# Kernel tuning notes

Measured on AMD Instinct MI355X. Metric: run time of the kernel, lower is better.

Reference implementation:

```python
import jax, jax.numpy as jnp
import numpy as np

N_INST = 50000
D_IN, D_HID, D_ATT = 1024, 512, 256  # size_dict['small']
N_ENS = 4
N_CLS = 2
CB_SIZE = 256
BETA = 0.25
TOP_K = 1


def setup_inputs() -> dict:
    key = jax.random.key(0)
    ks = jax.random.split(key, 9)
    h = jax.random.normal(ks[0], (N_INST, D_IN), dtype=jnp.float32)
    fc_W = jax.random.normal(ks[1], (D_IN, D_HID), dtype=jnp.float32) * (1.0 / np.sqrt(D_IN))
    fc_b = jnp.zeros((D_HID,), dtype=jnp.float32)
    Ua = jax.random.normal(ks[2], (N_ENS, D_HID, D_ATT), dtype=jnp.float32) * (1.0 / np.sqrt(D_HID))
    Ub = jax.random.normal(ks[3], (N_ENS, D_HID, D_ATT), dtype=jnp.float32) * (1.0 / np.sqrt(D_HID))
    Uc = jax.random.normal(ks[4], (N_ENS, D_ATT, 1), dtype=jnp.float32) * (1.0 / np.sqrt(D_ATT))
    cls_W = jax.random.normal(ks[5], (D_HID, N_CLS), dtype=jnp.float32) * (1.0 / np.sqrt(D_HID))
    cls_b = jnp.zeros((N_CLS,), dtype=jnp.float32)
    codebook = jax.random.normal(ks[6], (CB_SIZE, D_HID), dtype=jnp.float32)
    return {"h": h, "fc_W": fc_W, "fc_b": fc_b, "Ua": Ua, "Ub": Ub,
            "Uc": Uc, "cls_W": cls_W, "cls_b": cls_b, "codebook": codebook}


def _vector_quantization(M, codebook):
    # NOTE: original code uses +2*matmul (sign bug in torch source); kept faithful.
    dist = (jnp.sum(M * M, axis=1, keepdims=True)
            + jnp.sum(codebook * codebook, axis=1)
            + 2.0 * (M @ codebook.T))                      # [1, CB]
    inds = jnp.argmin(dist, axis=1)                        # [1]
    one_hot = jax.nn.one_hot(inds, CB_SIZE, dtype=M.dtype)  # [1, CB]
    q = one_hot @ codebook                                  # [1, D_HID]
    commitment = jnp.mean((jax.lax.stop_gradient(q) - M) ** 2)
    embedding = jnp.mean((q - jax.lax.stop_gradient(M)) ** 2)
    vq_loss = commitment * BETA + embedding
    q_st = M + jax.lax.stop_gradient(q - M)  # straight-through (unused downstream)
    return vq_loss, q_st


def reference(h, fc_W, fc_b, Ua, Ub, Uc, cls_W, cls_b, codebook):
    # fc + ReLU: [n, D_HID]
    x = jax.nn.relu(h @ fc_W + fc_b)
    # gated batch-ensemble attention (ensemble dim n=4 broadcast)
    xe = jnp.broadcast_to(x[None], (N_ENS, x.shape[0], D_HID))
    a = jnp.tanh(jnp.einsum('ndk,nkl->ndl', xe, Ua))         # [4, n, D_ATT]
    b = jax.nn.sigmoid(jnp.einsum('ndk,nkl->ndl', xe, Ub))   # [4, n, D_ATT]
    A = jnp.einsum('ndk,nkl->ndl', a * b, Uc).sum(0)          # [n, 1]
    A = jax.nn.sigmoid(A.T)                                   # [1, n]
    M = (A @ x) / jnp.sum(A)                                  # [1, D_HID]
    vq_loss, _M_code = _vector_quantization(M, codebook)
    logits = M @ cls_W + cls_b                                # [1, N_CLS]
    y_probs = jax.nn.softmax(logits, axis=1)
    _, top_idx = jax.lax.top_k(y_probs[:, 1], TOP_K)          # [1]
    top_instance = logits[top_idx]                            # [1, N_CLS]
    Y_hat = jnp.argmax(top_instance, axis=1)[:, None]         # [1, 1] int
    Y_prob = jax.nn.softmax(top_instance, axis=1)
    return (top_instance, Y_prob, Y_hat, vq_loss, y_probs, A)
```

## Files before the change

kernel.cpp:

```cpp
#include <hip/hip_runtime.h>
#include <hip/hip_bf16.h>
#include <math.h>

typedef __bf16 bf16_t;
typedef __bf16 bf16x8 __attribute__((ext_vector_type(8)));
typedef float  f32x4  __attribute__((ext_vector_type(4)));

#define MINST 50000

typedef const __attribute__((address_space(1))) void* gas1_t;
typedef __attribute__((address_space(3))) void* las3_t;
__device__ __forceinline__ void gload16(const void* g, const void* l){
  __builtin_amdgcn_global_load_lds((gas1_t)g, (las3_t)l, 16, 0, 0);
}

__device__ __forceinline__ float fast_sigmoid(float x){
  return __fdividef(1.f, 1.f + __expf(-x));
}
__device__ __forceinline__ float fast_tanh(float x){
  float e = __expf(2.f*x);
  return 1.f - __fdividef(2.f, e + 1.f);
}

__global__ void prep_wt(const float* __restrict__ W, bf16_t* __restrict__ WT){
  int idx = blockIdx.x*256 + threadIdx.x;
  if (idx >= 512*1024) return;
  int n = idx >> 10, k = idx & 1023;
  WT[idx] = (bf16_t)W[k*512 + n];
}

__global__ void prep_uab(const float* __restrict__ Ua, const float* __restrict__ Ub,
                         bf16_t* __restrict__ UabT){
  int idx = blockIdx.x*256 + threadIdx.x;
  if (idx >= 2048*512) return;
  int c = idx >> 9, k = idx & 511;
  int s = c & 1, t = c >> 1;
  int n = t >> 8, l = t & 255;
  const float* src = s ? Ub : Ua;
  UabT[idx] = (bf16_t)src[(n*512 + k)*256 + l];
}

__global__ void zero_ws_k(float* __restrict__ Alogit, float* __restrict__ Mbuf){
  int i = blockIdx.x*256 + threadIdx.x;
  if (i < MINST) Alogit[i] = 0.f;
  if (i < 513)   Mbuf[i]  = 0.f;
}

template<int EPI, int K, int NBY>
__global__ __launch_bounds__(256, 2)
void gemm_k(const void* __restrict__ Ap, const bf16_t* __restrict__ Bp, int M,
            const float* __restrict__ bias, bf16_t* __restrict__ Xout,
            const float* __restrict__ Uc, float* __restrict__ Alogit)
{
  __shared__ bf16_t As[(EPI==0?1:2)][128*32] __attribute__((aligned(16)));
  __shared__ bf16_t Bs[2][128*32] __attribute__((aligned(16)));

  const int tid  = threadIdx.x;
  const int lane = tid & 63;
  const int w    = tid >> 6;
  const int wr   = w >> 1;
  const int wc   = w & 1;

  const int nwg = gridDim.x;
  const int q = nwg >> 3, r = nwg & 7;
  const int x = blockIdx.x & 7, pos = blockIdx.x >> 3;
  const int logical = (x < r ? x*(q+1) : r*(q+1) + (x-r)*q) + pos;
  const int m0 = (logical / NBY) * 128;
  const int n0 = (logical % NBY) * 128;

  const f32x4 fzero = {0.f, 0.f, 0.f, 0.f};
  f32x4 acc[4][4];
#pragma unroll
  for (int m = 0; m < 4; ++m)
#pragma unroll
    for (int n = 0; n < 4; ++n) acc[m][n] = fzero;

  const int srow = lane >> 2;
  const int schk = (lane & 3) * 8;
  const bf16_t* bsrc0 = Bp + (size_t)(n0 + w*32 + srow)*K + schk;
  const bf16_t* bsrc1 = bsrc0 + (size_t)16*K;

  auto stageB = [&](int buf, int k0){
    gload16(bsrc0 + k0, &Bs[buf][(w*32     )*32]);
    gload16(bsrc1 + k0, &Bs[buf][(w*32 + 16)*32]);
  };

  const bf16_t* asrc0 = (const bf16_t*)Ap + (size_t)(m0 + w*32 + srow)*K + schk;
  const bf16_t* asrc1 = asrc0 + (size_t)16*K;
  auto stageA1 = [&](int buf, int k0){
    gload16(asrc0 + k0, &As[buf][(w*32     )*32]);
    gload16(asrc1 + k0, &As[buf][(w*32 + 16)*32]);
  };

  const int a_row  = tid >> 1;
  const int a_half = tid & 1;
  f32x4 sAf[4];
  auto loadA0 = [&](int k0){
    const float* A = (const float*)Ap;
    int gr = m0 + a_row;
    if (gr < M) {
      const f32x4* p = (const f32x4*)(A + (size_t)gr*K + k0 + a_half*16);
      sAf[0]=p[0]; sAf[1]=p[1]; sAf[2]=p[2]; sAf[3]=p[3];
    } else {
      sAf[0]=fzero; sAf[1]=fzero; sAf[2]=fzero; sAf[3]=fzero;
    }
  };
  auto writeA0 = [&](){
    bf16x8 lo, hi;
#pragma unroll
    for (int j = 0; j < 4; ++j) {
      lo[j]   = (bf16_t)sAf[0][j];
      lo[4+j] = (bf16_t)sAf[1][j];
      hi[j]   = (bf16_t)sAf[2][j];
      hi[4+j] = (bf16_t)sAf[3][j];
    }
    *(bf16x8*)&As[0][a_row*32 + a_half*16    ] = lo;
    *(bf16x8*)&As[0][a_row*32 + a_half*16 + 8] = hi;
  };

  const int fr = lane & 15;
  const int kh = lane >> 4;
  constexpr int NT = K / 32;

  if constexpr (EPI == 0) {
    loadA0(0);
    stageB(0, 0);
#pragma unroll 4
    for (int kt = 0; kt < NT; ++kt) {
      const int cur = kt & 1;
      __syncthreads();
      writeA0();
      __syncthreads();
      if (kt + 1 < NT) { loadA0((kt+1)*32); stageB(cur^1, (kt+1)*32); }
      bf16x8 a[4], b[4];
#pragma unroll
      for (int m = 0; m < 4; ++m)
        a[m] = *(const bf16x8*)&As[0][(wr*64 + m*16 + fr)*32 + kh*8];
#pragma unroll
      for (int n = 0; n < 4; ++n)
        b[n] = *(const bf16x8*)&Bs[cur][(wc*64 + n*16 + fr)*32 + kh*8];
#pragma unroll
      for (int m = 0; m < 4; ++m)
#pragma unroll
        for (int n = 0; n < 4; ++n)
          acc[m][n] = __builtin_amdgcn_mfma_f32_16x16x32_bf16(a[m], b[n], acc[m][n], 0, 0, 0);
    }
  } else {
    stageA1(0, 0);
    stageB(0, 0);
#pragma unroll 4
    for (int kt = 0; kt < NT; ++kt) {
      const int cur = kt & 1;
      __syncthreads();
      if (kt + 1 < NT) { stageA1(cur^1, (kt+1)*32); stageB(cur^1, (kt+1)*32); }
      bf16x8 a[4], b[4];
#pragma unroll
      for (int m = 0; m < 4; ++m)
        a[m] = *(const bf16x8*)&As[cur][(wr*64 + m*16 + fr)*32 + kh*8];
#pragma unroll
      for (int n = 0; n < 4; ++n)
        b[n] = *(const bf16x8*)&Bs[cur][(wc*64 + n*16 + fr)*32 + kh*8];
#pragma unroll
      for (int m = 0; m < 4; ++m)
#pragma unroll
        for (int n = 0; n < 4; ++n)
          acc[m][n] = __builtin_amdgcn_mfma_f32_16x16x32_bf16(a[m], b[n], acc[m][n], 0, 0, 0);
    }
  }

  const int rg = lane >> 4;
  if constexpr (EPI == 0) {
#pragma unroll
    for (int n = 0; n < 4; ++n) {
      int col = n0 + wc*64 + n*16 + fr;
      float bv = bias[col];
#pragma unroll
      for (int m = 0; m < 4; ++m)
#pragma unroll
        for (int rr = 0; rr < 4; ++rr) {
          int row = m0 + wr*64 + m*16 + rg*4 + rr;
          if (row < M) {
            float v = acc[m][n][rr] + bv;
            Xout[(size_t)row*512 + col] = (bf16_t)(v > 0.f ? v : 0.f);
          }
        }
    }
  } else {
    float gacc[4][4];
#pragma unroll
    for (int m = 0; m < 4; ++m)
#pragma unroll
      for (int rr = 0; rr < 4; ++rr) gacc[m][rr] = 0.f;
    const bool even = (lane & 1) == 0;
#pragma unroll
    for (int n = 0; n < 4; ++n) {
      int col = n0 + wc*64 + n*16 + fr;
      float ucv = Uc[col >> 1];
#pragma unroll
      for (int m = 0; m < 4; ++m)
#pragma unroll
        for (int rr = 0; rr < 4; ++rr) {
          float v = acc[m][n][rr];
          float tv = even ? fast_tanh(v) : fast_sigmoid(v);
          float pv = __shfl_xor(tv, 1);
          gacc[m][rr] += tv * pv * ucv;
        }
    }
#pragma unroll
    for (int m = 0; m < 4; ++m)
#pragma unroll
      for (int rr = 0; rr < 4; ++rr) {
        float s = gacc[m][rr];
        s += __shfl_xor(s, 1);
        s += __shfl_xor(s, 2);
        s += __shfl_xor(s, 4);
        s += __shfl_xor(s, 8);
        if (fr == 0) {
          int row = m0 + wr*64 + m*16 + rg*4 + rr;
          if (row < M) atomicAdd(&Alogit[row], 0.5f * s);
        }
      }
  }
}

__global__ void a_final(const float* __restrict__ Alogit, float* __restrict__ outA,
                        float* __restrict__ sumA){
  int i = blockIdx.x*256 + threadIdx.x;
  float a = 0.f;
  if (i < MINST) { a = fast_sigmoid(Alogit[i]); outA[i] = a; }
  float s = a;
#pragma unroll
  for (int o = 1; o < 64; o <<= 1) s += __shfl_xor(s, o);
  __shared__ float wsum[4];
  int lane = threadIdx.x & 63, w = threadIdx.x >> 6;
  if (lane == 0) wsum[w] = s;
  __syncthreads();
  if (threadIdx.x == 0) atomicAdd(sumA, wsum[0]+wsum[1]+wsum[2]+wsum[3]);
}

__global__ void m_reduce(const bf16_t* __restrict__ Xb, const float* __restrict__ Aout,
                         float* __restrict__ Mbuf){
  int t = threadIdx.x;
  int c0 = (t & 63) * 8;
  float acc[8];
#pragma unroll
  for (int j = 0; j < 8; ++j) acc[j] = 0.f;
  for (int r = blockIdx.x*4 + (t>>6); r < MINST; r += gridDim.x*4) {
    float a = Aout[r];
    bf16x8 xv = *(const bf16x8*)(Xb + (size_t)r*512 + c0);
#pragma unroll
    for (int j = 0; j < 8; ++j) acc[j] += a * (float)xv[j];
  }
#pragma unroll
  for (int j = 0; j < 8; ++j) atomicAdd(&Mbuf[c0 + j], acc[j]);
}

__device__ __forceinline__ float block_sum256(float v, float* red){
  int t = threadIdx.x;
  red[t] = v; __syncthreads();
  for (int s = 128; s > 0; s >>= 1) {
    if (t < s) red[t] += red[t+s];
    __syncthreads();
  }
  float rr = red[0];
  __syncthreads();
  return rr;
}

__global__ __launch_bounds__(256)
void finalize_k(const float* __restrict__ Mbuf, const float* __restrict__ cb,
                const float* __restrict__ clsW, const float* __restrict__ clsb,
                float* __restrict__ dout)
{
  __shared__ float Mn[512];
  __shared__ float red[256];
  __shared__ float dist[256];
  __shared__ int   idxs[256];
  __shared__ int   indS;
  int t = threadIdx.x;
  float sA = Mbuf[512];
  Mn[t]     = Mbuf[t]     / sA;
  Mn[t+256] = Mbuf[t+256] / sA;
  __syncthreads();
  float msq_p = Mn[t]*Mn[t] + Mn[t+256]*Mn[t+256];
  float Msq = block_sum256(msq_p, red);

  const float* cbr = cb + t*512;
  float cs = 0.f, dt = 0.f;
  for (int k = 0; k < 512; k += 4) {
    f32x4 c = *(const f32x4*)(cbr + k);
    cs += c[0]*c[0] + c[1]*c[1] + c[2]*c[2] + c[3]*c[3];
    dt += Mn[k]*c[0] + Mn[k+1]*c[1] + Mn[k+2]*c[2] + Mn[k+3]*c[3];
  }
  dist[t] = Msq + cs + 2.f*dt;
  idxs[t] = t;
  __syncthreads();
  for (int s = 128; s > 0; s >>= 1) {
    if (t < s && dist[t+s] < dist[t]) { dist[t] = dist[t+s]; idxs[t] = idxs[t+s]; }
    __syncthreads();
  }
  if (t == 0) indS = idxs[0];
  __syncthreads();

  const float* qv = cb + (size_t)indS*512;
  float d0 = qv[t]     - Mn[t];
  float d1 = qv[t+256] - Mn[t+256];
  float vqs = block_sum256(d0*d0 + d1*d1, red);
  float vq_loss = 1.25f * (vqs / 512.f);

  float p0 = Mn[t]*clsW[t*2]   + Mn[t+256]*clsW[(t+256)*2];
  float p1 = Mn[t]*clsW[t*2+1] + Mn[t+256]*clsW[(t+256)*2+1];
  float l0 = block_sum256(p0, red);
  float l1 = block_sum256(p1, red);

  if (t == 0) {
    l0 += clsb[0]; l1 += clsb[1];
    float mx = fmaxf(l0, l1);
    float e0 = __expf(l0 - mx), e1 = __expf(l1 - mx);
    float si = e0 + e1;
    float y0 = e0 / si, y1 = e1 / si;
    int yhat = (l1 > l0) ? 1 : 0;
    dout[0] = l0; dout[1] = l1;
    dout[2] = y0; dout[3] = y1;
    dout[4] = (float)yhat;
    dout[5] = vq_loss;
    dout[6] = y0; dout[7] = y1;
  }
}

extern "C" void kernel_launch(void* const* d_in, const int* in_sizes, int n_in,
                              void* d_out, int out_size, void* d_ws, size_t ws_size,
                              hipStream_t stream) {
  const float* h    = (const float*)d_in[0];
  const float* fcW  = (const float*)d_in[1];
  const float* fcb  = (const float*)d_in[2];
  const float* Ua   = (const float*)d_in[3];
  const float* Ub   = (const float*)d_in[4];
  const float* Uc   = (const float*)d_in[5];
  const float* clsW = (const float*)d_in[6];
  const float* clsb = (const float*)d_in[7];
  const float* cbk  = (const float*)d_in[8];
  float* out = (float*)d_out;

  char* ws = (char*)d_ws;
  bf16_t* Xb     = (bf16_t*)ws;
  bf16_t* WT     = (bf16_t*)(ws + 51200000);
  bf16_t* UabT   = (bf16_t*)(ws + 52248576);
  float*  Alogit = (float*)(ws + 54345728);
  float*  Mbuf   = (float*)(ws + 54545728);

  const int M = MINST;

  prep_wt <<<2048, 256, 0, stream>>>(fcW, WT);
  prep_uab<<<4096, 256, 0, stream>>>(Ua, Ub, UabT);
  zero_ws_k<<<196, 256, 0, stream>>>(Alogit, Mbuf);

  gemm_k<0,1024,4><<<1564, 256, 0, stream>>>(h, WT, M, fcb, Xb, nullptr, nullptr);
  gemm_k<1, 512,16><<<6256, 256, 0, stream>>>(Xb, UabT, M, nullptr, nullptr, Uc, Alogit);

  a_final <<<196, 256, 0, stream>>>(Alogit, out + 8, Mbuf + 512);
  m_reduce<<<128, 256, 0, stream>>>(Xb, out + 8, Mbuf);
  finalize_k<<<1, 256, 0, stream>>>(Mbuf, cbk, clsW, clsb, out);
}
```

Measured before the change: 507.1 us.

## Use 64-wide K tiles with XOR-swizzled LDS layout in GEMM kernels

Doubles the K-step of each shared-memory tile from 32 to 64, halving the number of loop iterations and barriers, and applies an XOR swizzle on 16-byte chunks to avoid LDS bank conflicts when reading fragments. For the attention GEMM (EPI!=0) it replaces double buffering with a single buffer that is read into registers and then refilled, and it drops the unroll pragmas. The risk is more registers for doubled fragments and less load/compute overlap in the single-buffered path.

```diff
diff --git a/kernel.cpp b/kernel.cpp
--- a/kernel.cpp
+++ b/kernel.cpp
@@ -52,8 +52,9 @@
             const float* __restrict__ bias, bf16_t* __restrict__ Xout,
             const float* __restrict__ Uc, float* __restrict__ Alogit)
 {
-  __shared__ bf16_t As[(EPI==0?1:2)][128*32] __attribute__((aligned(16)));
-  __shared__ bf16_t Bs[2][128*32] __attribute__((aligned(16)));
+  constexpr int NBUFB = (EPI==0 ? 2 : 1);
+  __shared__ bf16_t As[128*64] __attribute__((aligned(16)));
+  __shared__ bf16_t Bs[NBUFB][128*64] __attribute__((aligned(16)));
 
   const int tid  = threadIdx.x;
   const int lane = tid & 63;
@@ -75,96 +76,109 @@
 #pragma unroll
     for (int n = 0; n < 4; ++n) acc[m][n] = fzero;
 
-  const int srow = lane >> 2;
-  const int schk = (lane & 3) * 8;
-  const bf16_t* bsrc0 = Bp + (size_t)(n0 + w*32 + srow)*K + schk;
-  const bf16_t* bsrc1 = bsrc0 + (size_t)16*K;
-
-  auto stageB = [&](int buf, int k0){
-    gload16(bsrc0 + k0, &Bs[buf][(w*32     )*32]);
-    gload16(bsrc1 + k0, &Bs[buf][(w*32 + 16)*32]);
-  };
-
-  const bf16_t* asrc0 = (const bf16_t*)Ap + (size_t)(m0 + w*32 + srow)*K + schk;
-  const bf16_t* asrc1 = asrc0 + (size_t)16*K;
-  auto stageA1 = [&](int buf, int k0){
-    gload16(asrc0 + k0, &As[buf][(w*32     )*32]);
-    gload16(asrc1 + k0, &As[buf][(w*32 + 16)*32]);
+  const int sR = lane >> 3;
+  const int sC = (lane & 7) ^ sR;
+
+  auto stageB = [&](int kt, int buf){
+#pragma unroll
+    for (int j = 0; j < 4; ++j) {
+      int rL = w*32 + j*8;
+      gload16(Bp + (size_t)(n0 + rL + sR)*K + kt*64 + sC*8, &Bs[buf][rL*64]);
+    }
+  };
+  auto stageA1 = [&](int kt){
+    const bf16_t* Ab = (const bf16_t*)Ap;
+#pragma unroll
+    for (int j = 0; j < 4; ++j) {
+      int rL = w*32 + j*8;
+      gload16(Ab + (size_t)(m0 + rL + sR)*K + kt*64 + sC*8, &As[rL*64]);
+    }
   };
 
   const int a_row  = tid >> 1;
   const int a_half = tid & 1;
-  f32x4 sAf[4];
-  auto loadA0 = [&](int k0){
+  f32x4 sAf[8];
+  auto loadA0 = [&](int kt){
     const float* A = (const float*)Ap;
     int gr = m0 + a_row;
     if (gr < M) {
-      const f32x4* p = (const f32x4*)(A + (size_t)gr*K + k0 + a_half*16);
-      sAf[0]=p[0]; sAf[1]=p[1]; sAf[2]=p[2]; sAf[3]=p[3];
+      const f32x4* p = (const f32x4*)(A + (size_t)gr*K + kt*64 + a_half*32);
+#pragma unroll
+      for (int j = 0; j < 8; ++j) sAf[j] = p[j];
     } else {
-      sAf[0]=fzero; sAf[1]=fzero; sAf[2]=fzero; sAf[3]=fzero;
+#pragma unroll
+      for (int j = 0; j < 8; ++j) sAf[j] = fzero;
     }
   };
   auto writeA0 = [&](){
-    bf16x8 lo, hi;
 #pragma unroll
     for (int j = 0; j < 4; ++j) {
-      lo[j]   = (bf16_t)sAf[0][j];
-      lo[4+j] = (bf16_t)sAf[1][j];
-      hi[j]   = (bf16_t)sAf[2][j];
-      hi[4+j] = (bf16_t)sAf[3][j];
-    }
-    *(bf16x8*)&As[0][a_row*32 + a_half*16    ] = lo;
-    *(bf16x8*)&As[0][a_row*32 + a_half*16 + 8] = hi;
+      bf16x8 v;
+#pragma unroll
+      for (int e = 0; e < 4; ++e) { v[e] = (bf16_t)sAf[2*j][e]; v[4+e] = (bf16_t)sAf[2*j+1][e]; }
+      int c = (a_half*4 + j) ^ (a_row & 7);
+      *(bf16x8*)&As[a_row*64 + c*8] = v;
+    }
   };
 
   const int fr = lane & 15;
   const int kh = lane >> 4;
-  constexpr int NT = K / 32;
+  auto readFrags = [&](int buf, bf16x8 (&a)[4][2], bf16x8 (&b)[4][2]){
+#pragma unroll
+    for (int m = 0; m < 4; ++m){
+      int R = wr*64 + m*16 + fr;
+#pragma unroll
+      for (int ks = 0; ks < 2; ++ks){
+        int c = ((ks<<2)|kh) ^ (R & 7);
+        a[m][ks] = *(const bf16x8*)&As[R*64 + c*8];
+      }
+    }
+#pragma unroll
+    for (int n = 0; n < 4; ++n){
+      int R = wc*64 + n*16 + fr;
+#pragma unroll
+      for (int ks = 0; ks < 2; ++ks){
+        int c = ((ks<<2)|kh) ^ (R & 7);
+        b[n][ks] = *(const bf16x8*)&Bs[buf][R*64 + c*8];
+      }
+    }
+  };
+
+  constexpr int NT = K / 64;
 
   if constexpr (EPI == 0) {
-    loadA0(0);
-    stageB(0, 0);
-#pragma unroll 4
+    loadA0(0); stageB(0, 0);
     for (int kt = 0; kt < NT; ++kt) {
       const int cur = kt & 1;
       __syncthreads();
       writeA0();
       __syncthreads();
-      if (kt + 1 < NT) { loadA0((kt+1)*32); stageB(cur^1, (kt+1)*32); }
-      bf16x8 a[4], b[4];
-#pragma unroll
-      for (int m = 0; m < 4; ++m)
-        a[m] = *(const bf16x8*)&As[0][(wr*64 + m*16 + fr)*32 + kh*8];
-#pragma unroll
-      for (int n = 0; n < 4; ++n)
-        b[n] = *(const bf16x8*)&Bs[cur][(wc*64 + n*16 + fr)*32 + kh*8];
-#pragma unroll
-      for (int m = 0; m < 4; ++m)
-#pragma unroll
-        for (int n = 0; n < 4; ++n)
-          acc[m][n] = __builtin_amdgcn_mfma_f32_16x16x32_bf16(a[m], b[n], acc[m][n], 0, 0, 0);
+      if (kt + 1 < NT) { loadA0(kt+1); stageB(kt+1, cur^1); }
+      bf16x8 a[4][2], b[4][2];
+      readFrags(cur, a, b);
+#pragma unroll
+      for (int ks = 0; ks < 2; ++ks)
+#pragma unroll
+        for (int m = 0; m < 4; ++m)
+#pragma unroll
+          for (int n = 0; n < 4; ++n)
+            acc[m][n] = __builtin_amdgcn_mfma_f32_16x16x32_bf16(a[m][ks], b[n][ks], acc[m][n], 0, 0, 0);
     }
   } else {
-    stageA1(0, 0);
-    stageB(0, 0);
-#pragma unroll 4
+    stageA1(0); stageB(0, 0);
     for (int kt = 0; kt < NT; ++kt) {
-      const int cur = kt & 1;
       __syncthreads();
-      if (kt + 1 < NT) { stageA1(cur^1, (kt+1)*32); stageB(cur^1, (kt+1)*32); }
-      bf16x8 a[4], b[4];
-#pragma unroll
-      for (int m = 0; m < 4; ++m)
-        a[m] = *(const bf16x8*)&As[cur][(wr*64 + m*16 + fr)*32 + kh*8];
-#pragma unroll
-      for (int n = 0; n < 4; ++n)
-        b[n] = *(const bf16x8*)&Bs[cur][(wc*64 + n*16 + fr)*32 + kh*8];
-#pragma unroll
-      for (int m = 0; m < 4; ++m)
-#pragma unroll
-        for (int n = 0; n < 4; ++n)
-          acc[m][n] = __builtin_amdgcn_mfma_f32_16x16x32_bf16(a[m], b[n], acc[m][n], 0, 0, 0);
+      bf16x8 a[4][2], b[4][2];
+      readFrags(0, a, b);
+      __syncthreads();
+      if (kt + 1 < NT) { stageA1(kt+1); stageB(kt+1, 0); }
+#pragma unroll
+      for (int ks = 0; ks < 2; ++ks)
+#pragma unroll
+        for (int m = 0; m < 4; ++m)
+#pragma unroll
+          for (int n = 0; n < 4; ++n)
+            acc[m][n] = __builtin_amdgcn_mfma_f32_16x16x32_bf16(a[m][ks], b[n][ks], acc[m][n], 0, 0, 0);
     }
   }
 
```

After: 505.9 us. Within noise of the previous version (-0.3%).

## Split GEMM into specialized kernels with async fp32 A staging and swizzled LDS

Applied to the files above, without the earlier changes.

The templated GEMM is split into two kernels. The fc GEMM now streams fp32 activations straight into double-buffered LDS with global_load_lds and converts them to bf16 at fragment-read time, replacing the register load, convert and store path that needed two barriers per k-step. Both kernels get XOR-swizzled LDS layouts to cut bank conflicts, a single barrier per iteration, and higher occupancy hints (3 and 5 blocks per CU). The fp32 A tile doubles LDS use in the fc kernel and adds per-fragment conversion work, and the higher occupancy targets may raise register pressure.

```diff
diff --git a/kernel.cpp b/kernel.cpp
--- a/kernel.cpp
+++ b/kernel.cpp
@@ -46,14 +46,13 @@
   if (i < 513)   Mbuf[i]  = 0.f;
 }
 
-template<int EPI, int K, int NBY>
-__global__ __launch_bounds__(256, 2)
-void gemm_k(const void* __restrict__ Ap, const bf16_t* __restrict__ Bp, int M,
-            const float* __restrict__ bias, bf16_t* __restrict__ Xout,
-            const float* __restrict__ Uc, float* __restrict__ Alogit)
+__global__ __launch_bounds__(256, 3)
+void gemm_fc(const float* __restrict__ Ap, const bf16_t* __restrict__ Bp, int M,
+             const float* __restrict__ bias, bf16_t* __restrict__ Xout)
 {
-  __shared__ bf16_t As[(EPI==0?1:2)][128*32] __attribute__((aligned(16)));
-  __shared__ bf16_t Bs[2][128*32] __attribute__((aligned(16)));
+  constexpr int K = 1024, NBY = 4, NT = K/32;
+  __shared__ float  Asf[2][128*32] __attribute__((aligned(16)));
+  __shared__ bf16_t Bs [2][128*32] __attribute__((aligned(16)));
 
   const int tid  = threadIdx.x;
   const int lane = tid & 63;
@@ -75,152 +74,184 @@
 #pragma unroll
     for (int n = 0; n < 4; ++n) acc[m][n] = fzero;
 
-  const int srow = lane >> 2;
-  const int schk = (lane & 3) * 8;
-  const bf16_t* bsrc0 = Bp + (size_t)(n0 + w*32 + srow)*K + schk;
-  const bf16_t* bsrc1 = bsrc0 + (size_t)16*K;
-
-  auto stageB = [&](int buf, int k0){
-    gload16(bsrc0 + k0, &Bs[buf][(w*32     )*32]);
-    gload16(bsrc1 + k0, &Bs[buf][(w*32 + 16)*32]);
+  const int sq8 = lane >> 3;
+  const int sc8 = (lane & 7) ^ sq8;
+  const float* aSrc[4];
+#pragma unroll
+  for (int j = 0; j < 4; ++j){
+    int srow = m0 + w*32 + j*8 + sq8;
+    if (srow > M-1) srow = M-1;
+    aSrc[j] = Ap + (size_t)srow*K + sc8*4;
+  }
+  const int sq4 = lane >> 2;
+  const int sc4 = (lane & 3) ^ ((sq4 + (sq4 >> 2)) & 3);
+  const bf16_t* bSrc[2];
+#pragma unroll
+  for (int j = 0; j < 2; ++j)
+    bSrc[j] = Bp + (size_t)(n0 + w*32 + j*16 + sq4)*K + sc4*8;
+
+  auto stage = [&](int kt, int buf){
+#pragma unroll
+    for (int j = 0; j < 4; ++j)
+      gload16(aSrc[j] + kt*32, &Asf[buf][(w*32 + j*8)*32]);
+#pragma unroll
+    for (int j = 0; j < 2; ++j)
+      gload16(bSrc[j] + kt*32, &Bs[buf][(w*32 + j*16)*32]);
   };
 
-  const bf16_t* asrc0 = (const bf16_t*)Ap + (size_t)(m0 + w*32 + srow)*K + schk;
-  const bf16_t* asrc1 = asrc0 + (size_t)16*K;
-  auto stageA1 = [&](int buf, int k0){
-    gload16(asrc0 + k0, &As[buf][(w*32     )*32]);
-    gload16(asrc1 + k0, &As[buf][(w*32 + 16)*32]);
-  };
-
-  const int a_row  = tid >> 1;
-  const int a_half = tid & 1;
-  f32x4 sAf[4];
-  auto loadA0 = [&](int k0){
-    const float* A = (const float*)Ap;
-    int gr = m0 + a_row;
-    if (gr < M) {
-      const f32x4* p = (const f32x4*)(A + (size_t)gr*K + k0 + a_half*16);
-      sAf[0]=p[0]; sAf[1]=p[1]; sAf[2]=p[2]; sAf[3]=p[3];
-    } else {
-      sAf[0]=fzero; sAf[1]=fzero; sAf[2]=fzero; sAf[3]=fzero;
+  const int fr = lane & 15;
+  const int kh = lane >> 4;
+  const int cb = (kh ^ ((fr + (fr >> 2)) & 3)) * 8;
+  const int ca0 = ((2*kh    ) ^ (fr & 7)) * 4;
+  const int ca1 = ((2*kh + 1) ^ (fr & 7)) * 4;
+
+  stage(0, 0);
+  __syncthreads();
+  for (int kt = 0; kt < NT; ++kt){
+    const int cur = kt & 1;
+    if (kt + 1 < NT) stage(kt+1, cur^1);
+    bf16x8 a[4], b[4];
+#pragma unroll
+    for (int m = 0; m < 4; ++m){
+      int R = wr*64 + m*16 + fr;
+      f32x4 lo = *(const f32x4*)&Asf[cur][R*32 + ca0];
+      f32x4 hi = *(const f32x4*)&Asf[cur][R*32 + ca1];
+#pragma unroll
+      for (int e = 0; e < 4; ++e){ a[m][e] = (bf16_t)lo[e]; a[m][4+e] = (bf16_t)hi[e]; }
+    }
+#pragma unroll
+    for (int n = 0; n < 4; ++n)
+      b[n] = *(const bf16x8*)&Bs[cur][(wc*64 + n*16 + fr)*32 + cb];
+#pragma unroll
+    for (int m = 0; m < 4; ++m)
+#pragma unroll
+      for (int n = 0; n < 4; ++n)
+        acc[m][n] = __builtin_amdgcn_mfma_f32_16x16x32_bf16(a[m], b[n], acc[m][n], 0, 0, 0);
+    __syncthreads();
+  }
+
+  const int rg = lane >> 4;
+#pragma unroll
+  for (int n = 0; n < 4; ++n) {
+    int col = n0 + wc*64 + n*16 + fr;
+    float bv = bias[col];
+#pragma unroll
+    for (int m = 0; m < 4; ++m)
+#pragma unroll
+      for (int rr = 0; rr < 4; ++rr) {
+        int row = m0 + wr*64 + m*16 + rg*4 + rr;
+        if (row < M) {
+          float v = acc[m][n][rr] + bv;
+          Xout[(size_t)row*512 + col] = (bf16_t)(v > 0.f ? v : 0.f);
+        }
+      }
+  }
+}
+
+__global__ __launch_bounds__(256, 5)
+void gemm_att(const bf16_t* __restrict__ Xb, const bf16_t* __restrict__ Bp, int M,
+              const float* __restrict__ Uc, float* __restrict__ Alogit)
+{
+  constexpr int K = 512, NBY = 16, NT = K/32;
+  __shared__ bf16_t As[2][128*32] __attribute__((aligned(16)));
+  __shared__ bf16_t Bs[2][128*32] __attribute__((aligned(16)));
+
+  const int tid  = threadIdx.x;
+  const int lane = tid & 63;
+  const int w    = tid >> 6;
+  const int wr   = w >> 1;
+  const int wc   = w & 1;
+
+  const int nwg = gridDim.x;
+  const int q = nwg >> 3, r = nwg & 7;
+  const int x = blockIdx.x & 7, pos = blockIdx.x >> 3;
+  const int logical = (x < r ? x*(q+1) : r*(q+1) + (x-r)*q) + pos;
+  const int m0 = (logical / NBY) * 128;
+  const int n0 = (logical % NBY) * 128;
+
+  const f32x4 fzero = {0.f, 0.f, 0.f, 0.f};
+  f32x4 acc[4][4];
+#pragma unroll
+  for (int m = 0; m < 4; ++m)
+#pragma unroll
+    for (int n = 0; n < 4; ++n) acc[m][n] = fzero;
+
+  const int sq = lane >> 2;
+  const int sc = (lane & 3) ^ ((sq + (sq >> 2)) & 3);
+  const bf16_t* aSrc[2]; const bf16_t* bSrc[2];
+#pragma unroll
+  for (int j = 0; j < 2; ++j){
+    int rL = w*32 + j*16;
+    aSrc[j] = Xb + (size_t)(m0 + rL + sq)*K + sc*8;
+    bSrc[j] = Bp + (size_t)(n0 + rL + sq)*K + sc*8;
+  }
+  auto stage = [&](int kt, int buf){
+#pragma unroll
+    for (int j = 0; j < 2; ++j){
+      gload16(aSrc[j] + kt*32, &As[buf][(w*32 + j*16)*32]);
+      gload16(bSrc[j] + kt*32, &Bs[buf][(w*32 + j*16)*32]);
     }
   };
-  auto writeA0 = [&](){
-    bf16x8 lo, hi;
-#pragma unroll
-    for (int j = 0; j < 4; ++j) {
-      lo[j]   = (bf16_t)sAf[0][j];
-      lo[4+j] = (bf16_t)sAf[1][j];
-      hi[j]   = (bf16_t)sAf[2][j];
-      hi[4+j] = (bf16_t)sAf[3][j];
-    }
-    *(bf16x8*)&As[0][a_row*32 + a_half*16    ] = lo;
-    *(bf16x8*)&As[0][a_row*32 + a_half*16 + 8] = hi;
-  };
 
   const int fr = lane & 15;
   const int kh = lane >> 4;
-  constexpr int NT = K / 32;
-
-  if constexpr (EPI == 0) {
-    loadA0(0);
-    stageB(0, 0);
-#pragma unroll 4
-    for (int kt = 0; kt < NT; ++kt) {
-      const int cur = kt & 1;
-      __syncthreads();
-      writeA0();
-      __syncthreads();
-      if (kt + 1 < NT) { loadA0((kt+1)*32); stageB(cur^1, (kt+1)*32); }
-      bf16x8 a[4], b[4];
-#pragma unroll
-      for (int m = 0; m < 4; ++m)
-        a[m] = *(const bf16x8*)&As[0][(wr*64 + m*16 + fr)*32 + kh*8];
+  const int cs = (kh ^ ((fr + (fr >> 2)) & 3)) * 8;
+
+  stage(0, 0);
+  __syncthreads();
+  for (int kt = 0; kt < NT; ++kt){
+    const int cur = kt & 1;
+    if (kt + 1 < NT) stage(kt+1, cur^1);
+    bf16x8 a[4], b[4];
+#pragma unroll
+    for (int m = 0; m < 4; ++m)
+      a[m] = *(const bf16x8*)&As[cur][(wr*64 + m*16 + fr)*32 + cs];
+#pragma unroll
+    for (int n = 0; n < 4; ++n)
+      b[n] = *(const bf16x8*)&Bs[cur][(wc*64 + n*16 + fr)*32 + cs];
+#pragma unroll
+    for (int m = 0; m < 4; ++m)
 #pragma unroll
       for (int n = 0; n < 4; ++n)
-        b[n] = *(const bf16x8*)&Bs[cur][(wc*64 + n*16 + fr)*32 + kh*8];
-#pragma unroll
-      for (int m = 0; m < 4; ++m)
-#pragma unroll
-        for (int n = 0; n < 4; ++n)
-          acc[m][n] = __builtin_amdgcn_mfma_f32_16x16x32_bf16(a[m], b[n], acc[m][n], 0, 0, 0);
+        acc[m][n] = __builtin_amdgcn_mfma_f32_16x16x32_bf16(a[m], b[n], acc[m][n], 0, 0, 0);
+    __syncthreads();
+  }
+
+  const int rg = lane >> 4;
+  float gacc[4][4];
+#pragma unroll
+  for (int m = 0; m < 4; ++m)
+#pragma unroll
+    for (int rr = 0; rr < 4; ++rr) gacc[m][rr] = 0.f;
+  const bool even = (lane & 1) == 0;
+#pragma unroll
+  for (int n = 0; n < 4; ++n) {
+    int col = n0 + wc*64 + n*16 + fr;
+    float ucv = Uc[col >> 1];
+#pragma unroll
+    for (int m = 0; m < 4; ++m)
+#pragma unroll
+      for (int rr = 0; rr < 4; ++rr) {
+        float v = acc[m][n][rr];
+        float tv = even ? fast_tanh(v) : fast_sigmoid(v);
+        float pv = __shfl_xor(tv, 1);
+        gacc[m][rr] += tv * pv * ucv;
+      }
+  }
+#pragma unroll
+  for (int m = 0; m < 4; ++m)
+#pragma unroll
+    for (int rr = 0; rr < 4; ++rr) {
+      float s = gacc[m][rr];
+      s += __shfl_xor(s, 1);
+      s += __shfl_xor(s, 2);
+      s += __shfl_xor(s, 4);
+      s += __shfl_xor(s, 8);
+      if (fr == 0) {
+        int row = m0 + wr*64 + m*16 + rg*4 + rr;
+        if (row < M) atomicAdd(&Alogit[row], 0.5f * s);
+      }
     }
-  } else {
-    stageA1(0, 0);
-    stageB(0, 0);
-#pragma unroll 4
-    for (int kt = 0; kt < NT; ++kt) {
-      const int cur = kt & 1;
-      __syncthreads();
-      if (kt + 1 < NT) { stageA1(cur^1, (kt+1)*32); stageB(cur^1, (kt+1)*32); }
-      bf16x8 a[4], b[4];
-#pragma unroll
-      for (int m = 0; m < 4; ++m)
-        a[m] = *(const bf16x8*)&As[cur][(wr*64 + m*16 + fr)*32 + kh*8];
-#pragma unroll
-      for (int n = 0; n < 4; ++n)
-        b[n] = *(const bf16x8*)&Bs[cur][(wc*64 + n*16 + fr)*32 + kh*8];
-#pragma unroll
-      for (int m = 0; m < 4; ++m)
-#pragma unroll
-        for (int n = 0; n < 4; ++n)
-          acc[m][n] = __builtin_amdgcn_mfma_f32_16x16x32_bf16(a[m], b[n], acc[m][n], 0, 0, 0);
-    }
-  }
-
-  const int rg = lane >> 4;
-  if constexpr (EPI == 0) {
-#pragma unroll
-    for (int n = 0; n < 4; ++n) {
-      int col = n0 + wc*64 + n*16 + fr;
-      float bv = bias[col];
-#pragma unroll
-      for (int m = 0; m < 4; ++m)
-#pragma unroll
-        for (int rr = 0; rr < 4; ++rr) {
-          int row = m0 + wr*64 + m*16 + rg*4 + rr;
-          if (row < M) {
-            float v = acc[m][n][rr] + bv;
-            Xout[(size_t)row*512 + col] = (bf16_t)(v > 0.f ? v : 0.f);
-          }
-        }
-    }
-  } else {
-    float gacc[4][4];
-#pragma unroll
-    for (int m = 0; m < 4; ++m)
-#pragma unroll
-      for (int rr = 0; rr < 4; ++rr) gacc[m][rr] = 0.f;
-    const bool even = (lane & 1) == 0;
-#pragma unroll
-    for (int n = 0; n < 4; ++n) {
-      int col = n0 + wc*64 + n*16 + fr;
-      float ucv = Uc[col >> 1];
-#pragma unroll
-      for (int m = 0; m < 4; ++m)
-#pragma unroll
-        for (int rr = 0; rr < 4; ++rr) {
-          float v = acc[m][n][rr];
-          float tv = even ? fast_tanh(v) : fast_sigmoid(v);
-          float pv = __shfl_xor(tv, 1);
-          gacc[m][rr] += tv * pv * ucv;
-        }
-    }
-#pragma unroll
-    for (int m = 0; m < 4; ++m)
-#pragma unroll
-      for (int rr = 0; rr < 4; ++rr) {
-        float s = gacc[m][rr];
-        s += __shfl_xor(s, 1);
-        s += __shfl_xor(s, 2);
-        s += __shfl_xor(s, 4);
-        s += __shfl_xor(s, 8);
-        if (fr == 0) {
-          int row = m0 + wr*64 + m*16 + rg*4 + rr;
-          if (row < M) atomicAdd(&Alogit[row], 0.5f * s);
-        }
-      }
-  }
 }
 
 __global__ void a_final(const float* __restrict__ Alogit, float* __restrict__ outA,
@@ -355,8 +386,8 @@
   prep_uab<<<4096, 256, 0, stream>>>(Ua, Ub, UabT);
   zero_ws_k<<<196, 256, 0, stream>>>(Alogit, Mbuf);
 
-  gemm_k<0,1024,4><<<1564, 256, 0, stream>>>(h, WT, M, fcb, Xb, nullptr, nullptr);
-  gemm_k<1, 512,16><<<6256, 256, 0, stream>>>(Xb, UabT, M, nullptr, nullptr, Uc, Alogit);
+  gemm_fc<<<1564, 256, 0, stream>>>(h, WT, M, fcb, Xb);
+  gemm_att<<<6256, 256, 0, stream>>>(Xb, UabT, M, Uc, Alogit);
 
   a_final <<<196, 256, 0, stream>>>(Alogit, out + 8, Mbuf + 512);
   m_reduce<<<128, 256, 0, stream>>>(Xb, out + 8, Mbuf);
```

Measured after the change: 671.6 us. 1.32x slower.
